# Optimization experiments

Measured on AMD Instinct MI355X. Metric: run time of the kernel, lower is better.

## Reference

```python
import jax, jax.numpy as jnp
import numpy as np

N = 20000
NEG_SLOPE = 0.2


def gatv2_layer(x, src, dst, edge_attr, Wl, bl, Wr, br, We, att, bias, H, C):
    """PyG GATv2Conv: add self-loops (edge_attr fill='mean'), gather-score-softmax-aggregate."""
    n = x.shape[0]
    E = src.shape[0]
    # --- add self loops, self-loop edge_attr = mean of incoming edge_attr per node ---
    ea_sum = jax.ops.segment_sum(edge_attr, dst, num_segments=n)
    deg = jax.ops.segment_sum(jnp.ones((E, 1), x.dtype), dst, num_segments=n)
    ea_loop = ea_sum / jnp.maximum(deg, 1.0)
    loop = jnp.arange(n)
    src_a = jnp.concatenate([src, loop])
    dst_a = jnp.concatenate([dst, loop])
    ea = jnp.concatenate([edge_attr, ea_loop], axis=0)
    # --- linear projections ---
    xl = (x @ Wl + bl).reshape(n, H, C)   # source-side features
    xr = (x @ Wr + br).reshape(n, H, C)   # target-side features
    e = (ea @ We).reshape(-1, H, C)       # edge features
    # --- per-edge GATv2 attention score ---
    m = xl[src_a] + xr[dst_a] + e                          # [E', H, C]
    s = jnp.sum(jax.nn.leaky_relu(m, NEG_SLOPE) * att, -1)  # [E', H]
    # --- softmax over incoming edges of each target node ---
    smax = jax.ops.segment_max(s, dst_a, num_segments=n)
    ex = jnp.exp(s - smax[dst_a])
    denom = jax.ops.segment_sum(ex, dst_a, num_segments=n)
    alpha = ex / (denom[dst_a] + 1e-16)                    # [E', H]
    # --- aggregate messages (alpha * x_l[src]) ---
    out = jax.ops.segment_sum(alpha[..., None] * xl[src_a], dst_a, num_segments=n)
    return out.reshape(n, H * C) + bias


def setup_inputs() -> dict:
    key = jax.random.key(0)
    ks = jax.random.split(key, 20)
    F, HID, H1, A = 128, 32, 8, 128
    E = 640000
    d = {}
    d["x"] = jax.random.normal(ks[0], (N, F), jnp.float32)
    d["edge_index"] = jax.random.randint(ks[1], (2, E), 0, N, jnp.int32).astype(jnp.int64)
    d["edge_attr"] = jax.random.normal(ks[2], (E, 1), jnp.float32)
    # layer 1 params (in=F, out=HID, heads=H1)
    d["W1l"] = jax.random.normal(ks[3], (F, H1 * HID), jnp.float32) * 0.05
    d["b1l"] = jnp.zeros((H1 * HID,), jnp.float32)
    d["W1r"] = jax.random.normal(ks[4], (F, H1 * HID), jnp.float32) * 0.05
    d["b1r"] = jnp.zeros((H1 * HID,), jnp.float32)
    d["We1"] = jax.random.normal(ks[5], (1, H1 * HID), jnp.float32) * 0.05
    d["att1"] = jax.random.normal(ks[6], (H1, HID), jnp.float32) * 0.05
    d["bias1"] = jnp.zeros((H1 * HID,), jnp.float32)
    # layer 2 params (in=H1*HID, out=A, heads=1)
    d["W2l"] = jax.random.normal(ks[7], (H1 * HID, A), jnp.float32) * 0.05
    d["b2l"] = jnp.zeros((A,), jnp.float32)
    d["W2r"] = jax.random.normal(ks[8], (H1 * HID, A), jnp.float32) * 0.05
    d["b2r"] = jnp.zeros((A,), jnp.float32)
    d["We2"] = jax.random.normal(ks[9], (1, A), jnp.float32) * 0.05
    d["att2"] = jax.random.normal(ks[10], (1, A), jnp.float32) * 0.05
    d["bias2"] = jnp.zeros((A,), jnp.float32)
    d["alpha"] = jnp.array(0.0, jnp.float32)
    return d


def reference(x, edge_index, edge_attr, W1l, b1l, W1r, b1r, We1, att1, bias1,
              W2l, b2l, W2r, b2r, We2, att2, bias2, alpha):
    src, dst = edge_index[0], edge_index[1]
    h = jax.nn.relu(gatv2_layer(x, src, dst, edge_attr, W1l, b1l, W1r, b1r,
                                We1, att1, bias1, H=8, C=32))
    h = jax.nn.relu(gatv2_layer(h, src, dst, edge_attr, W2l, b2l, W2r, b2r,
                                We2, att2, bias2, H=1, C=128))
    pooled = jnp.mean(h, axis=0, keepdims=True)  # global_mean_pool, single graph -> [1, A]
    return jax.nn.softmax(pooled, axis=1), jax.nn.sigmoid(alpha)
```

## Files before the change

kernel.cpp:

```cpp
#include <hip/hip_runtime.h>
#include <math.h>

#define NEG_SLOPE 0.2f
#define LOG2E 1.4426950408889634f

typedef __attribute__((ext_vector_type(8))) short short8;
typedef __attribute__((ext_vector_type(4))) float f32x4;
typedef __attribute__((ext_vector_type(2))) float v2f;

__device__ __forceinline__ int imin(int a, int b) { return a < b ? a : b; }

__device__ __forceinline__ unsigned int f2bf(float f) {
    unsigned int u = __float_as_uint(f);
    return (u + 0x7fffu + ((u >> 16) & 1u)) >> 16;
}
__device__ __forceinline__ float fast_exp2(float x) {
#if __has_builtin(__builtin_amdgcn_exp2f)
    return __builtin_amdgcn_exp2f(x);
#else
    return exp2f(x);
#endif
}
__device__ __forceinline__ unsigned char f2fp8(float v) {
    return (unsigned char)(__builtin_amdgcn_cvt_pk_fp8_f32(v, v, 0, false) & 0xff);
}
template <int CTRL>
__device__ __forceinline__ float dpp_add(float v) {
    int t = __builtin_amdgcn_update_dpp(0, __float_as_int(v), CTRL, 0xF, 0xF, true);
    return v + __int_as_float(t);
}
__device__ __forceinline__ v2f pk_fma(v2f a, v2f b, v2f c) {
    v2f d;
    asm("v_pk_fma_f32 %0, %1, %2, %3" : "=v"(d) : "v"(a), "v"(b), "v"(c));
    return d;
}
__device__ __forceinline__ v2f pk_add(v2f a, v2f b) {
    v2f d;
    asm("v_pk_add_f32 %0, %1, %2" : "=v"(d) : "v"(a), "v"(b));
    return d;
}

__global__ void fused_prep(const int* __restrict__ ei, const float* __restrict__ ea,
                           unsigned long long* __restrict__ hist, int E,
                           const float* __restrict__ x, unsigned short* __restrict__ xb, int nF4,
                           const float* __restrict__ W1l, const float* __restrict__ W1r,
                           const float* __restrict__ W2l, const float* __restrict__ W2r,
                           const float* __restrict__ b1l, const float* __restrict__ b1r,
                           const float* __restrict__ b2l, const float* __restrict__ b2r,
                           unsigned short* __restrict__ Wt1, unsigned short* __restrict__ Wt2,
                           float* __restrict__ b1cat, float* __restrict__ b2cat,
                           int F, int HC1, int HC2) {
    int i = blockIdx.x * blockDim.x + threadIdx.x;
    if (i < E) {
        int d = ei[E + i];
        long long fx = (long long)__float2int_rn(ea[i] * 65536.0f);
        unsigned long long v = ((unsigned long long)fx << 32) | 1ull;
        atomicAdd(&hist[(size_t)d * 8], v);
        return;
    }
    int j = i - E;
    if (j < nF4) {
        float4 v = ((const float4*)x)[j];
        uint2 r;
        r.x = f2bf(v.x) | (f2bf(v.y) << 16);
        r.y = f2bf(v.z) | (f2bf(v.w) << 16);
        ((uint2*)xb)[j] = r;
        return;
    }
    int k = j - nF4;
    int S1 = F * HC1, S2 = HC1 * HC2;
    if (k < S1) {
        int kk = k / HC1, nn = k - kk * HC1;
        Wt1[(size_t)nn * F + kk] = (unsigned short)f2bf(W1l[k]);
    } else if (k < 2 * S1) {
        int m = k - S1;
        int kk = m / HC1, nn = m - kk * HC1;
        Wt1[(size_t)(HC1 + nn) * F + kk] = (unsigned short)f2bf(W1r[m]);
    } else if (k < 2 * S1 + S2) {
        int m = k - 2 * S1;
        int kk = m / HC2, nn = m - kk * HC2;
        Wt2[(size_t)nn * HC1 + kk] = (unsigned short)f2bf(W2l[m]);
    } else if (k < 2 * S1 + 2 * S2) {
        int m = k - 2 * S1 - S2;
        int kk = m / HC2, nn = m - kk * HC2;
        Wt2[(size_t)(HC2 + nn) * HC1 + kk] = (unsigned short)f2bf(W2r[m]);
    } else if (k < 2 * S1 + 2 * S2 + 2 * HC1) {
        int m = k - 2 * S1 - 2 * S2;
        b1cat[m] = (m < HC1) ? b1l[m] : b1r[m - HC1];
    } else if (k < 2 * S1 + 2 * S2 + 2 * HC1 + 2 * HC2) {
        int m = k - 2 * S1 - 2 * S2 - 2 * HC1;
        b2cat[m] = (m < HC2) ? b2l[m] : b2r[m - HC2];
    }
}

__global__ void scan_a(const unsigned long long* __restrict__ hist, int* __restrict__ bsum, int n) {
    __shared__ int wred[4];
    int base = blockIdx.x * 1024;
    int tid = threadIdx.x;
    int s = 0;
#pragma unroll
    for (int k = 0; k < 4; ++k) {
        int i = base + tid + k * 256;
        if (i < n) s += (int)(hist[(size_t)i * 8] & 0xffffffffull);
    }
#pragma unroll
    for (int off = 32; off > 0; off >>= 1) s += __shfl_xor(s, off, 64);
    if ((tid & 63) == 0) wred[tid >> 6] = s;
    __syncthreads();
    if (tid == 0) bsum[blockIdx.x] = wred[0] + wred[1] + wred[2] + wred[3];
}

__global__ void scan_c(const unsigned long long* __restrict__ hist,
                       const int* __restrict__ bsum, int* __restrict__ row_ptr,
                       int* __restrict__ wptr_pad, float* __restrict__ ea_loop,
                       int n, int B) {
    __shared__ int wtot[4];
    __shared__ int sh_base;
    int tid = threadIdx.x;
    int wid = tid >> 6, lane = tid & 63;
    int i0 = blockIdx.x * 1024 + tid * 4;
    int dcnt[4]; float esum[4];
#pragma unroll
    for (int k = 0; k < 4; ++k) {
        if (i0 + k < n) {
            unsigned long long h = hist[(size_t)(i0 + k) * 8];
            dcnt[k] = (int)(h & 0xffffffffull);
            esum[k] = (float)((int)(h >> 32)) * (1.0f / 65536.0f);
        } else { dcnt[k] = 0; esum[k] = 0.0f; }
    }
    int tsum = dcnt[0] + dcnt[1] + dcnt[2] + dcnt[3];
    int s = tsum;
#pragma unroll
    for (int off = 1; off < 64; off <<= 1) {
        int t = __shfl_up(s, off, 64);
        if (lane >= off) s += t;
    }
    if (lane == 63) wtot[wid] = s;
    if (tid < 64) {
        int v   = (tid < B) ? bsum[tid] : 0;
        int pre = (tid < (int)blockIdx.x) ? v : 0;
        int tot = v;
#pragma unroll
        for (int off = 32; off > 0; off >>= 1) {
            pre += __shfl_xor(pre, off, 64);
            tot += __shfl_xor(tot, off, 64);
        }
        if (tid == 0) {
            sh_base = pre;
            if (blockIdx.x == 0) row_ptr[n] = tot;
        }
    }
    __syncthreads();
    int wpre = 0;
#pragma unroll
    for (int k = 0; k < 4; ++k) if (k < wid) wpre += wtot[k];
    int pre = sh_base + wpre + (s - tsum);
    if (i0 < n) {
        int4 e;
        e.x = pre;
        e.y = pre + dcnt[0];
        e.z = e.y + dcnt[1];
        e.w = e.z + dcnt[2];
        *(int4*)(row_ptr + i0) = e;
        int ev[4] = { e.x, e.y, e.z, e.w };
        float4 el;
        el.x = esum[0] / fmaxf((float)dcnt[0], 1.0f);
        el.y = esum[1] / fmaxf((float)dcnt[1], 1.0f);
        el.z = esum[2] / fmaxf((float)dcnt[2], 1.0f);
        el.w = esum[3] / fmaxf((float)dcnt[3], 1.0f);
        *(float4*)(ea_loop + i0) = el;
#pragma unroll
        for (int k = 0; k < 4; ++k) wptr_pad[(size_t)(i0 + k) * 16] = ev[k];
    }
}

__global__ void edge_scatter(const int* __restrict__ ei, const float* __restrict__ ea,
                             int* __restrict__ wptr_pad, int2* __restrict__ spk, int E) {
    int e = blockIdx.x * blockDim.x + threadIdx.x;
    if (e < E) {
        int d = ei[E + e];
        int pos = atomicAdd(&wptr_pad[(size_t)d * 16], 1);
        spk[pos] = make_int2(ei[e], __float_as_int(ea[e]));
    }
}

template <bool OUT_FP8>
__global__ void __launch_bounds__(256)
gemm_bf16(const unsigned short* __restrict__ A, const unsigned short* __restrict__ Bt,
          const float* __restrict__ bias, void* __restrict__ Cv, void* __restrict__ Cv2,
          int split, int M, int N, int K) {
    __shared__ __attribute__((aligned(16))) unsigned short As[64 * 40];
    __shared__ __attribute__((aligned(16))) unsigned short Bs[64 * 40];
    int tid  = threadIdx.x;
    int wave = tid >> 6, lane = tid & 63;
    int m0 = blockIdx.x * 64, n0 = blockIdx.y * 64;
    int row = tid >> 2, kg = (tid & 3) * 8;

    f32x4 acc[4] = {};
    for (int kk = 0; kk < K; kk += 32) {
        int gm = m0 + row;
        uint4 av;
        if (gm < M) av = *(const uint4*)(A + (size_t)gm * K + kk + kg);
        else        av = make_uint4(0, 0, 0, 0);
        *(uint4*)&As[row * 40 + kg] = av;
        uint4 bv = *(const uint4*)(Bt + (size_t)(n0 + row) * K + kk + kg);
        *(uint4*)&Bs[row * 40 + kg] = bv;
        __syncthreads();
        short8 a = *(const short8*)&As[(wave * 16 + (lane & 15)) * 40 + (lane >> 4) * 8];
#pragma unroll
        for (int g = 0; g < 4; ++g) {
            short8 b = *(const short8*)&Bs[(g * 16 + (lane & 15)) * 40 + (lane >> 4) * 8];
            acc[g] = __builtin_amdgcn_mfma_f32_16x16x32_bf16(a, b, acc[g], 0, 0, 0);
        }
        __syncthreads();
    }
#pragma unroll
    for (int g = 0; g < 4; ++g) {
        int col = n0 + g * 16 + (lane & 15);
        float bs = bias[col];
#pragma unroll
        for (int r = 0; r < 4; ++r) {
            int grow = m0 + wave * 16 + (lane >> 4) * 4 + r;
            if (grow < M) {
                float val = acc[g][r] + bs;
                if constexpr (OUT_FP8) {
                    unsigned char c = f2fp8(val);
                    if (col < split) ((unsigned char*)Cv)[(size_t)grow * split + col] = c;
                    else             ((unsigned char*)Cv2)[(size_t)grow * split + (col - split)] = c;
                } else {
                    ((unsigned short*)Cv)[(size_t)grow * N + col] = (unsigned short)f2bf(val);
                }
            }
        }
    }
}

template <int NV>
__device__ __forceinline__ void unp1(unsigned int u, v2f* xf) {
    xf[0] = __builtin_amdgcn_cvt_pk_f32_fp8(u, false);
    if constexpr (NV == 4) xf[1] = __builtin_amdgcn_cvt_pk_f32_fp8(u, true);
}
template <int G>
__device__ __forceinline__ float grp_reduce(float vs) {
    vs = dpp_add<0xB1>(vs);
    if constexpr (G >= 4)  vs = dpp_add<0x4E>(vs);
    if constexpr (G >= 8)  vs = dpp_add<0x141>(vs);
    if constexpr (G >= 16) vs = dpp_add<0x140>(vs);
    if constexpr (G >= 32) {
        int t = __builtin_amdgcn_ds_swizzle(__float_as_int(vs), 0x401F);
        vs += __int_as_float(t);
    }
    if constexpr (G >= 64) vs += __shfl_xor(vs, 32, 64);
    return vs;
}

template <int HC, int C, int OUT_MODE>
__global__ void __launch_bounds__(256)
gat_agg(const unsigned char* __restrict__ xl, const unsigned char* __restrict__ xr,
        const float* __restrict__ We, const float* __restrict__ att,
        const float* __restrict__ bias,
        const int* __restrict__ row_ptr, const int2* __restrict__ spk,
        const float* __restrict__ ea_loop,
        void* __restrict__ out, int n) {
    constexpr int NV = HC / 64;
    constexpr int NG = (NV + 1) / 2;
    constexpr int G  = C / NV;
    constexpr int SHIFT = (HC == 256) ? 8 : 7;
    constexpr float K23 = 2.0f / 3.0f;
    __shared__ float red[4][128];
    int wave = threadIdx.x >> 6;
    int lane = threadIdx.x & 63;
    int node = blockIdx.x * 4 + wave;
    bool active = node < n;
    if (OUT_MODE == 0 && !active) return;
    unsigned int lo = (unsigned int)lane * NV;

    float vout[NV];
#pragma unroll
    for (int j = 0; j < NV; ++j) vout[j] = 0.0f;

    if (active) {
        auto ldd = [&](const unsigned char* base, unsigned int off) -> unsigned int {
            if constexpr (NV == 4) return *(const unsigned int*)(base + off);
            else                   return (unsigned int)(*(const unsigned short*)(base + off));
        };
        auto gat = [&](int s) -> unsigned int {
            return ldd(xl, ((unsigned int)s << SHIFT) + lo);
        };
        auto W = [&](int2 s) -> float { return __int_as_float(s.y); };

        v2f xr2[NG], We2[NG], att62[NG], o2[NG];
        {
            v2f tmp[NG];
            unp1<NV>(ldd(xr, ((unsigned int)node << SHIFT) + lo), tmp);
#pragma unroll
            for (int g = 0; g < NG; ++g) xr2[g] = tmp[g];
        }
#pragma unroll
        for (int g = 0; g < NG; ++g) {
            We2[g]   = *(const v2f*)(We  + lo + 2 * g);
            v2f a    = *(const v2f*)(att + lo + 2 * g);
            att62[g] = a * (0.6f * LOG2E);
            o2[g]    = v2f{0.0f, 0.0f};
        }
        float l = 0.0f;

        int start = __builtin_amdgcn_readfirstlane(row_ptr[node]);
        int end   = __builtin_amdgcn_readfirstlane(row_ptr[node + 1]);
        float ea_l = ea_loop[node];

        auto process = [&](unsigned int du, float w) {
            v2f xf[NG];
            unp1<NV>(du, xf);
            v2f w2 = {w, w};
            v2f vs6 = {0.0f, 0.0f};
            float vs4 = 0.0f;
#pragma unroll
            for (int g = 0; g < NG; ++g) {
                v2f t  = pk_fma(w2, We2[g], xr2[g]);
                v2f mm = pk_add(xf[g], t);
                vs6 = pk_fma(att62[g], mm, vs6);
                vs4 = fmaf(fabsf(mm.x), att62[g].x, vs4);
                vs4 = fmaf(fabsf(mm.y), att62[g].y, vs4);
            }
            float vs = fmaf(K23, vs4, vs6.x + vs6.y);
            vs = grp_reduce<G>(vs);
            float pr = fast_exp2(vs);
            l += pr;
            v2f pr2 = {pr, pr};
#pragma unroll
            for (int g = 0; g < NG; ++g) o2[g] = pk_fma(xf[g], pr2, o2[g]);
        };

        process(gat(node), ea_l);

        int cnt = end - start;
        const int2* q = spk + start;

        if (cnt >= 6) {
            int2 t;
            t = q[0]; unsigned int g0 = gat(t.x); float w0 = W(t);
            t = q[1]; unsigned int g1 = gat(t.x); float w1 = W(t);
            t = q[2]; unsigned int g2 = gat(t.x); float w2 = W(t);
            t = q[3]; unsigned int g3 = gat(t.x); float w3 = W(t);
            t = q[4]; unsigned int g4 = gat(t.x); float w4 = W(t);
            t = q[5]; unsigned int g5 = gat(t.x); float w5 = W(t);
            int p = 0;
            for (; p + 12 <= cnt; p += 6) {
                process(g0, w0); t = q[p + 6];  g0 = gat(t.x); w0 = W(t);
                process(g1, w1); t = q[p + 7];  g1 = gat(t.x); w1 = W(t);
                process(g2, w2); t = q[p + 8];  g2 = gat(t.x); w2 = W(t);
                process(g3, w3); t = q[p + 9];  g3 = gat(t.x); w3 = W(t);
                process(g4, w4); t = q[p + 10]; g4 = gat(t.x); w4 = W(t);
                process(g5, w5); t = q[p + 11]; g5 = gat(t.x); w5 = W(t);
            }
            process(g0, w0); process(g1, w1); process(g2, w2);
            process(g3, w3); process(g4, w4); process(g5, w5);
            for (int k = p + 6; k < cnt; ++k) {
                t = q[k];
                process(gat(t.x), W(t));
            }
        } else {
            for (int k = 0; k < cnt; ++k) {
                int2 t = q[k];
                process(gat(t.x), W(t));
            }
        }

        float inv = 1.0f / (l + 1e-16f);
#pragma unroll
        for (int g = 0; g < NG; ++g) {
            v2f b = *(const v2f*)(bias + lo + 2 * g);
            vout[2 * g]     = fmaxf(o2[g].x * inv + b.x, 0.0f);
            vout[2 * g + 1] = fmaxf(o2[g].y * inv + b.y, 0.0f);
        }
        if constexpr (OUT_MODE == 0) {
            unsigned short* op = (unsigned short*)out + (size_t)node * HC + lo;
            if constexpr (NV == 4) {
                uint2 t;
                t.x = f2bf(vout[0]) | (f2bf(vout[1]) << 16);
                t.y = f2bf(vout[2]) | (f2bf(vout[3]) << 16);
                *(uint2*)op = t;
            } else {
                *(unsigned int*)op = f2bf(vout[0]) | (f2bf(vout[1]) << 16);
            }
        }
    }

    if constexpr (OUT_MODE == 1) {
#pragma unroll
        for (int j = 0; j < NV; ++j) red[wave][lo + j] = vout[j];
        __syncthreads();
        if (wave == 0) {
            int c = lane;
            float a = red[0][c] + red[1][c] + red[2][c] + red[3][c];
            float b = red[0][c + 64] + red[1][c + 64] + red[2][c + 64] + red[3][c + 64];
            float* pacc = (float*)out + (size_t)(blockIdx.x & 255) * 128;
            atomicAdd(&pacc[c], a);
            atomicAdd(&pacc[c + 64], b);
        }
    }
}

__global__ void __launch_bounds__(1024)
pool_final(const float* __restrict__ partial, int nb,
           const float* __restrict__ alpha_in,
           float* __restrict__ out, int n) {
    __shared__ float acc[8][128];
    __shared__ float red[4];
    int t = threadIdx.x & 127;
    int g = threadIdx.x >> 7;
    float s = 0.0f;
    for (int b = g; b < nb; b += 8) s += partial[b * 128 + t];
    acc[g][t] = s;
    __syncthreads();
    if (threadIdx.x < 128) {
        float tot = 0.0f;
#pragma unroll
        for (int k = 0; k < 8; ++k) tot += acc[k][t];
        float mean = tot / (float)n;
        float mx = mean;
#pragma unroll
        for (int off = 32; off > 0; off >>= 1) mx = fmaxf(mx, __shfl_xor(mx, off, 64));
        if ((t & 63) == 0) red[t >> 6] = mx;
        __syncthreads();
        mx = fmaxf(red[0], red[1]);
        float ex = __expf(mean - mx);
        float sm = ex;
#pragma unroll
        for (int off = 32; off > 0; off >>= 1) sm += __shfl_xor(sm, off, 64);
        if ((t & 63) == 0) red[2 + (t >> 6)] = sm;
        __syncthreads();
        sm = red[2] + red[3];
        out[t] = ex / sm;
        if (t == 0) out[128] = 1.0f / (1.0f + __expf(-alpha_in[0]));
    }
}

extern "C" void kernel_launch(void* const* d_in, const int* in_sizes, int n_in,
                              void* d_out, int out_size, void* d_ws, size_t ws_size,
                              hipStream_t stream) {
    const float* x    = (const float*)d_in[0];
    const int*   ei   = (const int*)d_in[1];
    const float* ea   = (const float*)d_in[2];
    const float* W1l  = (const float*)d_in[3];
    const float* b1l  = (const float*)d_in[4];
    const float* W1r  = (const float*)d_in[5];
    const float* b1r  = (const float*)d_in[6];
    const float* We1  = (const float*)d_in[7];
    const float* att1 = (const float*)d_in[8];
    const float* bias1= (const float*)d_in[9];
    const float* W2l  = (const float*)d_in[10];
    const float* b2l  = (const float*)d_in[11];
    const float* W2r  = (const float*)d_in[12];
    const float* b2r  = (const float*)d_in[13];
    const float* We2  = (const float*)d_in[14];
    const float* att2 = (const float*)d_in[15];
    const float* bias2= (const float*)d_in[16];
    const float* alpha= (const float*)d_in[17];
    float* out = (float*)d_out;

    const int F = 128, HC1 = 256, HC2 = 128;
    const int n = in_sizes[0] / F;
    const int E = in_sizes[1] / 2;
    const int B = (n + 1023) / 1024;

    char* ws = (char*)d_ws;
    size_t off = 0;
    auto alloc = [&](size_t bytes) { size_t p = off; off += (bytes + 255) & ~(size_t)255; return p; };

    unsigned long long* hist = (unsigned long long*)(ws + alloc((size_t)n * 8 * 8));
    int*   row_ptr = (int*)  (ws + alloc((size_t)(n + 1) * 4));
    int*   wptr    = (int*)  (ws + alloc((size_t)n * 16 * 4));
    float* ea_loop = (float*)(ws + alloc((size_t)n * 4));
    int*   bsum    = (int*)  (ws + alloc(64 * 4));
    int2*  spk     = (int2*) (ws + alloc((size_t)E * 8));
    unsigned short* xb   = (unsigned short*)(ws + alloc((size_t)n * F * 2));
    unsigned short* Wt1  = (unsigned short*)(ws + alloc((size_t)F * (2 * HC1) * 2));
    unsigned short* Wt2  = (unsigned short*)(ws + alloc((size_t)HC1 * (2 * HC2) * 2));
    float* b1cat   = (float*)(ws + alloc((size_t)2 * HC1 * 4));
    float* b2cat   = (float*)(ws + alloc((size_t)2 * HC2 * 4));
    unsigned char* xl1 = (unsigned char*)(ws + alloc((size_t)n * HC1));
    unsigned char* xr1 = (unsigned char*)(ws + alloc((size_t)n * HC1));
    unsigned short* h1  = (unsigned short*)(ws + alloc((size_t)n * HC1 * 2));
    float* partial = (float*)(ws + alloc((size_t)256 * 128 * 4));
    unsigned char* xl2 = xl1;
    unsigned char* xr2 = xr1;
    const int NB_SLOTS = 256;

    (void)hipMemsetAsync(hist, 0, (size_t)n * 8 * 8, stream);
    (void)hipMemsetAsync(partial, 0, (size_t)NB_SLOTS * 128 * 4, stream);

    int tb = 256;
    {
        int nF4  = n * F / 4;
        int WTOT = 2 * F * HC1 + 2 * HC1 * HC2 + 2 * HC1 + 2 * HC2;
        int total = E + nF4 + WTOT;
        fused_prep<<<(total + tb - 1) / tb, tb, 0, stream>>>(
            ei, ea, hist, E, x, xb, nF4,
            W1l, W1r, W2l, W2r, b1l, b1r, b2l, b2r,
            Wt1, Wt2, b1cat, b2cat, F, HC1, HC2);
    }
    scan_a<<<B, 256, 0, stream>>>(hist, bsum, n);
    scan_c<<<B, 256, 0, stream>>>(hist, bsum, row_ptr, wptr, ea_loop, n, B);
    edge_scatter<<<(E + tb - 1) / tb, tb, 0, stream>>>(ei, ea, wptr, spk, E);

    {
        dim3 grid((n + 63) / 64, (2 * HC1) / 64);
        gemm_bf16<true><<<grid, 256, 0, stream>>>(xb, Wt1, b1cat, xl1, xr1, HC1, n, 2 * HC1, F);
    }
    gat_agg<256, 32, 0><<<(n + 3) / 4, 256, 0, stream>>>(
        xl1, xr1, We1, att1, bias1, row_ptr, spk, ea_loop, h1, n);

    {
        dim3 grid((n + 63) / 64, (2 * HC2) / 64);
        gemm_bf16<true><<<grid, 256, 0, stream>>>(h1, Wt2, b2cat, xl2, xr2, HC2, n, 2 * HC2, HC1);
    }
    gat_agg<128, 128, 1><<<(n + 3) / 4, 256, 0, stream>>>(
        xl2, xr2, We2, att2, bias2, row_ptr, spk, ea_loop, partial, n);

    pool_final<<<1, 1024, 0, stream>>>(partial, NB_SLOTS, alpha, out, n);
}
```

Before: 274.8 us.

## Stream neighbor feature gathers through an LDS ring via global_load_lds

Replaces the six-deep register prefetch of gathered source-node rows in the aggregation kernel with asynchronous global-to-LDS loads into a per-wave 16-slot ring, kept eight loads ahead and synchronised with explicit vmcnt waits. The aim is deeper memory-latency hiding for the random gathers without tying up registers. Each lane always loads 4 bytes, so 128-byte rows overread into the next row, and the xl/xr buffers get extra padding to cover that. The index loads from the edge list also count toward vmcnt, so the hand-written wait and the compiler's own waits may interfere and weaken the overlap. The ring also adds 16 KB of shared memory per block, which may reduce occupancy.

```diff
diff --git a/kernel.cpp b/kernel.cpp
--- a/kernel.cpp
+++ b/kernel.cpp
@@ -7,6 +7,9 @@
 typedef __attribute__((ext_vector_type(8))) short short8;
 typedef __attribute__((ext_vector_type(4))) float f32x4;
 typedef __attribute__((ext_vector_type(2))) float v2f;
+
+typedef __attribute__((address_space(1))) unsigned int gu32;
+typedef __attribute__((address_space(3))) unsigned int lu32;
 
 __device__ __forceinline__ int imin(int a, int b) { return a < b ? a : b; }
 
@@ -267,6 +270,7 @@
     constexpr int G  = C / NV;
     constexpr int SHIFT = (HC == 256) ? 8 : 7;
     constexpr float K23 = 2.0f / 3.0f;
+    __shared__ __attribute__((aligned(16))) unsigned char ring[4][16 * 256];
     __shared__ float red[4][128];
     int wave = threadIdx.x >> 6;
     int lane = threadIdx.x & 63;
@@ -280,12 +284,12 @@
     for (int j = 0; j < NV; ++j) vout[j] = 0.0f;
 
     if (active) {
+        unsigned char* myring = ring[wave];
+        const unsigned char* gl = xl + (unsigned int)lane * 4;
+
         auto ldd = [&](const unsigned char* base, unsigned int off) -> unsigned int {
             if constexpr (NV == 4) return *(const unsigned int*)(base + off);
             else                   return (unsigned int)(*(const unsigned short*)(base + off));
-        };
-        auto gat = [&](int s) -> unsigned int {
-            return ldd(xl, ((unsigned int)s << SHIFT) + lo);
         };
         auto W = [&](int2 s) -> float { return __int_as_float(s.y); };
 
@@ -332,38 +336,30 @@
             for (int g = 0; g < NG; ++g) o2[g] = pk_fma(xf[g], pr2, o2[g]);
         };
 
-        process(gat(node), ea_l);
+        process(ldd(xl, ((unsigned int)node << SHIFT) + lo), ea_l);
 
         int cnt = end - start;
         const int2* q = spk + start;
 
-        if (cnt >= 6) {
-            int2 t;
-            t = q[0]; unsigned int g0 = gat(t.x); float w0 = W(t);
-            t = q[1]; unsigned int g1 = gat(t.x); float w1 = W(t);
-            t = q[2]; unsigned int g2 = gat(t.x); float w2 = W(t);
-            t = q[3]; unsigned int g3 = gat(t.x); float w3 = W(t);
-            t = q[4]; unsigned int g4 = gat(t.x); float w4 = W(t);
-            t = q[5]; unsigned int g5 = gat(t.x); float w5 = W(t);
-            int p = 0;
-            for (; p + 12 <= cnt; p += 6) {
-                process(g0, w0); t = q[p + 6];  g0 = gat(t.x); w0 = W(t);
-                process(g1, w1); t = q[p + 7];  g1 = gat(t.x); w1 = W(t);
-                process(g2, w2); t = q[p + 8];  g2 = gat(t.x); w2 = W(t);
-                process(g3, w3); t = q[p + 9];  g3 = gat(t.x); w3 = W(t);
-                process(g4, w4); t = q[p + 10]; g4 = gat(t.x); w4 = W(t);
-                process(g5, w5); t = q[p + 11]; g5 = gat(t.x); w5 = W(t);
-            }
-            process(g0, w0); process(g1, w1); process(g2, w2);
-            process(g3, w3); process(g4, w4); process(g5, w5);
-            for (int k = p + 6; k < cnt; ++k) {
-                t = q[k];
-                process(gat(t.x), W(t));
-            }
-        } else {
+        if (cnt > 0) {
+            auto issue = [&](int k2, int slot) {
+                int s = q[k2].x;
+                const unsigned char* gp = gl + ((size_t)(unsigned)s << SHIFT);
+                __builtin_amdgcn_global_load_lds((const gu32*)gp,
+                                                 (lu32*)(myring + slot * 256), 4, 0, 0);
+            };
+#pragma unroll
+            for (int j = 0; j < 8; ++j) issue(imin(j, cnt - 1), j);
             for (int k = 0; k < cnt; ++k) {
+                asm volatile("s_waitcnt vmcnt(7)" ::: "memory");
+                unsigned int du;
+                if constexpr (NV == 4)
+                    du = *(const unsigned int*)(myring + (k & 15) * 256 + lo);
+                else
+                    du = (unsigned int)*(const unsigned short*)(myring + (k & 15) * 256 + lo);
+                issue(imin(k + 8, cnt - 1), (k + 8) & 15);
                 int2 t = q[k];
-                process(gat(t.x), W(t));
+                process(du, W(t));
             }
         }
 
@@ -377,10 +373,12 @@
         if constexpr (OUT_MODE == 0) {
             unsigned short* op = (unsigned short*)out + (size_t)node * HC + lo;
             if constexpr (NV == 4) {
+                uint4* dummy;
                 uint2 t;
                 t.x = f2bf(vout[0]) | (f2bf(vout[1]) << 16);
                 t.y = f2bf(vout[2]) | (f2bf(vout[3]) << 16);
                 *(uint2*)op = t;
+                (void)dummy;
             } else {
                 *(unsigned int*)op = f2bf(vout[0]) | (f2bf(vout[1]) << 16);
             }
@@ -480,8 +478,8 @@
     unsigned short* Wt2  = (unsigned short*)(ws + alloc((size_t)HC1 * (2 * HC2) * 2));
     float* b1cat   = (float*)(ws + alloc((size_t)2 * HC1 * 4));
     float* b2cat   = (float*)(ws + alloc((size_t)2 * HC2 * 4));
-    unsigned char* xl1 = (unsigned char*)(ws + alloc((size_t)n * HC1));
-    unsigned char* xr1 = (unsigned char*)(ws + alloc((size_t)n * HC1));
+    unsigned char* xl1 = (unsigned char*)(ws + alloc((size_t)n * HC1 + 256));
+    unsigned char* xr1 = (unsigned char*)(ws + alloc((size_t)n * HC1 + 256));
     unsigned short* h1  = (unsigned short*)(ws + alloc((size_t)n * HC1 * 2));
     float* partial = (float*)(ws + alloc((size_t)256 * 128 * 4));
     unsigned char* xl2 = xl1;
```

Measured after the change: 294.8 us. 1.07x slower.

## Fuse edge scatter and layer-1 GEMM into one interleaved launch

Applied to the files above, without the earlier changes.

Merges the CSR edge-scatter kernel and the first-layer projection GEMM into a single kernel whose blocks alternate between scatter work and GEMM tiles. These two stages are independent, so running them concurrently lets the atomic-heavy, memory-bound scatter overlap with the MFMA GEMM, and one launch is saved. The cost is a larger kernel whose shared-memory and register footprint also applies to the scatter blocks, which may reduce their occupancy.

```diff
diff --git a/kernel.cpp b/kernel.cpp
--- a/kernel.cpp
+++ b/kernel.cpp
@@ -174,13 +174,69 @@
     }
 }
 
-__global__ void edge_scatter(const int* __restrict__ ei, const float* __restrict__ ea,
-                             int* __restrict__ wptr_pad, int2* __restrict__ spk, int E) {
-    int e = blockIdx.x * blockDim.x + threadIdx.x;
-    if (e < E) {
-        int d = ei[E + e];
-        int pos = atomicAdd(&wptr_pad[(size_t)d * 16], 1);
-        spk[pos] = make_int2(ei[e], __float_as_int(ea[e]));
+__global__ void __launch_bounds__(256)
+scat_gemm1(const int* __restrict__ ei, const float* __restrict__ ea,
+           int* __restrict__ wptr_pad, int2* __restrict__ spk, int E, int NS,
+           const unsigned short* __restrict__ A, const unsigned short* __restrict__ Bt,
+           const float* __restrict__ bias, unsigned char* __restrict__ Cv,
+           unsigned char* __restrict__ Cv2, int split, int M, int N, int K, int GB) {
+    __shared__ __attribute__((aligned(16))) unsigned short As[64 * 40];
+    __shared__ __attribute__((aligned(16))) unsigned short Bs[64 * 40];
+    int bid = blockIdx.x;
+    int nmin = imin(NS, GB);
+    bool is_scat;
+    int idx;
+    if (bid < 2 * nmin) { is_scat = !(bid & 1); idx = bid >> 1; }
+    else                { idx = bid - nmin;     is_scat = (NS > GB); }
+
+    if (is_scat) {
+        int e = idx * 256 + threadIdx.x;
+        if (e < E) {
+            int d = ei[E + e];
+            int pos = atomicAdd(&wptr_pad[(size_t)d * 16], 1);
+            spk[pos] = make_int2(ei[e], __float_as_int(ea[e]));
+        }
+        return;
+    }
+
+    int GY = N >> 6;
+    int bx = idx / GY, by = idx - bx * GY;
+    int tid  = threadIdx.x;
+    int wave = tid >> 6, lane = tid & 63;
+    int m0 = bx * 64, n0 = by * 64;
+    int row = tid >> 2, kg = (tid & 3) * 8;
+
+    f32x4 acc[4] = {};
+    for (int kk = 0; kk < K; kk += 32) {
+        int gm = m0 + row;
+        uint4 av;
+        if (gm < M) av = *(const uint4*)(A + (size_t)gm * K + kk + kg);
+        else        av = make_uint4(0, 0, 0, 0);
+        *(uint4*)&As[row * 40 + kg] = av;
+        uint4 bv = *(const uint4*)(Bt + (size_t)(n0 + row) * K + kk + kg);
+        *(uint4*)&Bs[row * 40 + kg] = bv;
+        __syncthreads();
+        short8 a = *(const short8*)&As[(wave * 16 + (lane & 15)) * 40 + (lane >> 4) * 8];
+#pragma unroll
+        for (int g = 0; g < 4; ++g) {
+            short8 b = *(const short8*)&Bs[(g * 16 + (lane & 15)) * 40 + (lane >> 4) * 8];
+            acc[g] = __builtin_amdgcn_mfma_f32_16x16x32_bf16(a, b, acc[g], 0, 0, 0);
+        }
+        __syncthreads();
+    }
+#pragma unroll
+    for (int g = 0; g < 4; ++g) {
+        int col = n0 + g * 16 + (lane & 15);
+        float bs = bias[col];
+#pragma unroll
+        for (int r = 0; r < 4; ++r) {
+            int grow = m0 + wave * 16 + (lane >> 4) * 4 + r;
+            if (grow < M) {
+                unsigned char c = f2fp8(acc[g][r] + bs);
+                if (col < split) Cv[(size_t)grow * split + col] = c;
+                else             Cv2[(size_t)grow * split + (col - split)] = c;
+            }
+        }
     }
 }
 
@@ -503,11 +559,15 @@
     }
     scan_a<<<B, 256, 0, stream>>>(hist, bsum, n);
     scan_c<<<B, 256, 0, stream>>>(hist, bsum, row_ptr, wptr, ea_loop, n, B);
-    edge_scatter<<<(E + tb - 1) / tb, tb, 0, stream>>>(ei, ea, wptr, spk, E);
 
     {
-        dim3 grid((n + 63) / 64, (2 * HC1) / 64);
-        gemm_bf16<true><<<grid, 256, 0, stream>>>(xb, Wt1, b1cat, xl1, xr1, HC1, n, 2 * HC1, F);
+        int NS = (E + 255) / 256;
+        int GB = ((n + 63) / 64) * ((2 * HC1) / 64);
+        int nmin = NS < GB ? NS : GB;
+        int grid = 2 * nmin + (NS > GB ? NS - GB : GB - NS);
+        scat_gemm1<<<grid, 256, 0, stream>>>(
+            ei, ea, wptr, spk, E, NS,
+            xb, Wt1, b1cat, xl1, xr1, HC1, n, 2 * HC1, F, GB);
     }
     gat_agg<256, 32, 0><<<(n + 3) / 4, 256, 0, stream>>>(
         xl1, xr1, We1, att1, bias1, row_ptr, spk, ea_loop, h1, n);
```

After: 258.6 us. 5.9% less time.
